# Performance work log

Hardware: AMD Instinct MI355X
Metric: run time of the kernel (lower is better)

Reference implementation:

```python
import jax, jax.numpy as jnp
import numpy as np

B, Q, K = 4, 1024, 2048
QDIM, MDIM, EDIM, H = 1024, 1024, 1024, 16
HD = EDIM // H

def setup_inputs() -> dict:
    key = jax.random.key(0)
    ks = jax.random.split(key, 7)
    s = lambda d: (1.0 / np.sqrt(d))
    return {
        'query': jax.random.normal(ks[0], (B, Q, QDIM), jnp.float32),
        'memory': jax.random.normal(ks[1], (B, K, MDIM), jnp.float32),
        'bias': jax.random.normal(ks[2], (B, K), jnp.float32),
        'Wq': jax.random.normal(ks[3], (QDIM, EDIM), jnp.float32) * s(QDIM),
        'Wk': jax.random.normal(ks[4], (MDIM, EDIM), jnp.float32) * s(MDIM),
        'Wv': jax.random.normal(ks[5], (MDIM, EDIM), jnp.float32) * s(MDIM),
        'Wo': jax.random.normal(ks[6], (EDIM, EDIM), jnp.float32) * s(EDIM),
    }

def reference(query, memory, bias, Wq, Wk, Wv, Wo):
    scale = HD ** -0.5
    # projections -> [B, H, Q/K, HD]
    q = (query @ Wq).reshape(B, Q, H, HD).transpose(0, 2, 1, 3)
    k = (memory @ Wk).reshape(B, K, H, HD).transpose(0, 2, 1, 3)
    v = (memory @ Wv).reshape(B, K, H, HD).transpose(0, 2, 1, 3)
    scores = jnp.einsum('bhqd,bhkd->bhqk', q, k) * scale
    scores = scores + bias[:, None, None, :]
    weights = jax.nn.softmax(scores, axis=-1)
    out = jnp.einsum('bhqk,bhkd->bhqd', weights, v)
    out = out.transpose(0, 2, 1, 3).reshape(B, Q, EDIM)
    return out @ Wo
```

## Files before the change

### kernel.cpp

```cpp
#include <hip/hip_runtime.h>
#include <cstdint>
#include <cstddef>

typedef unsigned short u16;
typedef __attribute__((ext_vector_type(8))) short bf16x8;
typedef __attribute__((ext_vector_type(4))) short bf16x4;
typedef __attribute__((ext_vector_type(4))) float f32x4;

#define B_  4
#define Q_  1024
#define K_  2048
#define E_  1024
#define H_  16
#define HD_ 64
#define LOG2E 1.4426950408889634f
#define M0_  16.0f

__device__ inline u16 f2bf(float f) {
  union { float f; uint32_t u; } x; x.f = f;
  return (u16)((x.u + 0x7fffu + ((x.u >> 16) & 1u)) >> 16);
}

__device__ inline short bfc(float f) {
  __bf16 h = (__bf16)f;
  return __builtin_bit_cast(short, h);
}

__device__ inline void gload16(const u16* g, void* l) {
  __builtin_amdgcn_global_load_lds((const __attribute__((address_space(1))) void*)g,
                                   (__attribute__((address_space(3))) void*)l, 16, 0, 0);
}

#define NQ8 (B_ * Q_ * E_ / 8)
#define NM8 (B_ * K_ * E_ / 8)
#define NBI (B_ * K_)
#define NPREP ((NQ8 + NM8 + NBI) / 256)
__global__ __launch_bounds__(256) void prep_all(const float* __restrict__ query,
                                                const float* __restrict__ memory,
                                                const float* __restrict__ bias,
                                                const float* W0, const float* W1,
                                                const float* W2, const float* W3,
                                                u16* __restrict__ qb,
                                                u16* __restrict__ mb,
                                                float* __restrict__ bias2,
                                                u16* T0, u16* T1, u16* T2, u16* T3) {
  __shared__ float t[64][65];
  int bid = blockIdx.x;
  if (bid < NPREP) {
    int i = bid * 256 + threadIdx.x;
    const float* src;
    u16* dst;
    if (i < NQ8) {
      src = query + (size_t)i * 8; dst = qb + (size_t)i * 8;
    } else if (i < NQ8 + NM8) {
      int j = i - NQ8;
      src = memory + (size_t)j * 8; dst = mb + (size_t)j * 8;
    } else {
      int j = i - (NQ8 + NM8);
      if (j < NBI) bias2[j] = bias[j] * LOG2E - M0_;
      return;
    }
    float4 a = *reinterpret_cast<const float4*>(src);
    float4 b = *reinterpret_cast<const float4*>(src + 4);
    union { u16 u[8]; uint4 v; } r;
    r.u[0] = f2bf(a.x); r.u[1] = f2bf(a.y); r.u[2] = f2bf(a.z); r.u[3] = f2bf(a.w);
    r.u[4] = f2bf(b.x); r.u[5] = f2bf(b.y); r.u[6] = f2bf(b.z); r.u[7] = f2bf(b.w);
    *reinterpret_cast<uint4*>(dst) = r.v;
  } else {
    int tb = bid - NPREP;
    int z = tb >> 8, xy = tb & 255;
    const float* W; u16* T;
    switch (z) {
      case 0: W = W0; T = T0; break;
      case 1: W = W1; T = T1; break;
      case 2: W = W2; T = T2; break;
      default: W = W3; T = T3; break;
    }
    int k0 = (xy & 15) * 64, n0 = (xy >> 4) * 64;
    int r = threadIdx.x >> 6, c = threadIdx.x & 63;
#pragma unroll
    for (int i = 0; i < 16; ++i)
      t[r + i * 4][c] = W[(size_t)(k0 + r + i * 4) * E_ + n0 + c];
    __syncthreads();
#pragma unroll
    for (int i = 0; i < 16; ++i)
      T[(size_t)(n0 + r + i * 4) * E_ + k0 + c] = f2bf(t[c][r + i * 4]);
  }
}

template <int MODE>
__device__ __forceinline__ void gemm_body(const u16* __restrict__ A,
                                          const u16* __restrict__ Bt,
                                          void* __restrict__ C,
                                          int M, int N, int Kc, int bx, int by,
                                          char* lds) {
  const int tid = threadIdx.x;
  const int w = tid >> 6, l = tid & 63;
  const int wr = w >> 1, wc = w & 1;
  const int lr = l & 15, lg = l >> 4;
  const int m0 = bx * 128, n0 = by * 128;

  const int e0g = tid * 8, e1g = e0g + 2048;
  const int row0 = e0g >> 5, row1 = e1g >> 5;
  const int lc0 = ((((e0g & 31) >> 3) ^ ((row0 >> 1) & 3)) * 8);
  const int lc1 = ((((e1g & 31) >> 3) ^ ((row1 >> 1) & 3)) * 8);
  const u16* Ar0 = A  + (size_t)(m0 + row0) * Kc + lc0;
  const u16* Ar1 = A  + (size_t)(m0 + row1) * Kc + lc1;
  const u16* Br0 = Bt + (size_t)(n0 + row0) * Kc + lc0;
  const u16* Br1 = Bt + (size_t)(n0 + row1) * Kc + lc1;
  const int d0 = tid * 16, d1 = d0 + 4096;

  const int ck = (lg ^ ((lr >> 1) & 3)) * 16;
  int aofs = (wr * 64 + lr) * 64 + ck;
  int bofs = 16384 + (wc * 64 + lr) * 64 + ck;

  f32x4 acc[4][4];
#pragma unroll
  for (int mt = 0; mt < 4; ++mt)
#pragma unroll
    for (int nt = 0; nt < 4; ++nt)
      acc[mt][nt] = (f32x4){0.f, 0.f, 0.f, 0.f};

  gload16(Ar0, lds + d0);
  gload16(Ar1, lds + d1);
  gload16(Br0, lds + 16384 + d0);
  gload16(Br1, lds + 16384 + d1);
  __syncthreads();

  const int NI = Kc >> 5;
  for (int ki = 0; ki < NI; ++ki) {
    if (ki + 1 < NI) {
      const int nb = ((ki & 1) ^ 1) * 8192;
      const int kk = (ki + 1) * 32;
      gload16(Ar0 + kk, lds + nb + d0);
      gload16(Ar1 + kk, lds + nb + d1);
      gload16(Br0 + kk, lds + 16384 + nb + d0);
      gload16(Br1 + kk, lds + 16384 + nb + d1);
    }

    bf16x8 a[4], b[4];
#pragma unroll
    for (int mt = 0; mt < 4; ++mt)
      a[mt] = *reinterpret_cast<const bf16x8*>(lds + aofs + mt * 1024);
#pragma unroll
    for (int nt = 0; nt < 4; ++nt)
      b[nt] = *reinterpret_cast<const bf16x8*>(lds + bofs + nt * 1024);
    __builtin_amdgcn_s_setprio(1);
#pragma unroll
    for (int mt = 0; mt < 4; ++mt)
#pragma unroll
      for (int nt = 0; nt < 4; ++nt)
        acc[mt][nt] = __builtin_amdgcn_mfma_f32_16x16x32_bf16(a[mt], b[nt], acc[mt][nt], 0, 0, 0);
    __builtin_amdgcn_s_setprio(0);

    aofs ^= 8192; bofs ^= 8192;
    __syncthreads();
  }

#pragma unroll
  for (int mt = 0; mt < 4; ++mt) {
#pragma unroll
    for (int nt = 0; nt < 4; ++nt) {
      int col = n0 + wc * 64 + nt * 16 + lr;
#pragma unroll
      for (int j = 0; j < 4; ++j) {
        int row = m0 + wr * 64 + mt * 16 + lg * 4 + j;
        float v = acc[mt][nt][j];
        if (MODE == 0) {
          ((float*)C)[(size_t)row * N + col] = v;
        } else if (MODE == 1) {
          ((u16*)C)[(size_t)row * N + col] = f2bf(v);
        } else if (MODE == 3) {
          ((u16*)C)[(size_t)row * N + col] = f2bf(v * (0.125f * LOG2E));
        } else {
          ((u16*)C)[((size_t)((col >> 11) * 16 + (row >> 6)) * 64 + (row & 63)) * 2048 + (col & 2047)] = f2bf(v);
        }
      }
    }
  }
}

__global__ __launch_bounds__(256) void gemm_out(const u16* __restrict__ A,
                                                const u16* __restrict__ Bt,
                                                void* __restrict__ C,
                                                int M, int N, int Kc) {
  __shared__ uint4 lds4[2048];
  int d = blockIdx.x;
  int bid = (d & 7) * 32 + (d >> 3);
  gemm_body<0>(A, Bt, C, M, N, Kc, bid >> 3, bid & 7, (char*)lds4);
}

__global__ __launch_bounds__(256) void proj_fused(const u16* __restrict__ qb,
                                                  const u16* __restrict__ mb,
                                                  const u16* __restrict__ wqt,
                                                  const u16* __restrict__ wkt,
                                                  const u16* __restrict__ wvt,
                                                  u16* __restrict__ qproj,
                                                  u16* __restrict__ kproj,
                                                  u16* __restrict__ vt) {
  __shared__ uint4 lds4[2048];
  char* lds = (char*)lds4;
  int d = blockIdx.x;
  int bid = (d & 7) * 160 + (d >> 3);
  if (bid < 256) {
    gemm_body<3>(qb, wqt, qproj, B_ * Q_, E_, E_, bid >> 3, bid & 7, lds);
  } else if (bid < 768) {
    int i = bid - 256;
    gemm_body<1>(mb, wkt, kproj, B_ * K_, E_, E_, i >> 3, i & 7, lds);
  } else {
    int i = bid - 768;
    gemm_body<2>(wvt, mb, vt, E_, B_ * K_, E_, i & 7, i >> 3, lds);
  }
}

__global__ __launch_bounds__(256, 4) void attn_kernel(const u16* __restrict__ qp,
                                                      const u16* __restrict__ kp,
                                                      const u16* __restrict__ vT,
                                                      const float* __restrict__ bias2,
                                                      u16* __restrict__ out) {
  __shared__ uint4 lds4[2048];
  char* ldsb = (char*)lds4;

  const int blk = blockIdx.x;
  const int hg = blk & 63, qt = blk >> 6;
  const int b = hg >> 4, h = hg & 15;
  const int tid = threadIdx.x;
  const int w = tid >> 6, l = tid & 63;
  const int lr = l & 15, lg = l >> 4;

  bf16x8 qfrag[2];
#pragma unroll
  for (int ks = 0; ks < 2; ++ks)
    qfrag[ks] = *reinterpret_cast<const bf16x8*>(
        qp + (size_t)(b * Q_ + qt * 64 + w * 16 + lr) * E_ + h * 64 + ks * 32 + lg * 8);

  f32x4 O[4];
  f32x4 Osum = (f32x4){0.f, 0.f, 0.f, 0.f};
#pragma unroll
  for (int ht = 0; ht < 4; ++ht) O[ht] = (f32x4){0.f, 0.f, 0.f, 0.f};
  const float* bias_b = bias2 + (size_t)b * K_;
  const u16* kbase = kp + (size_t)b * K_ * E_ + h * 64;
  const u16* vbase = vT + (size_t)(b * H_ + h) * HD_ * K_;

  const bf16x4 ones = {(short)0x3F80, (short)0x3F80, (short)0x3F80, (short)0x3F80};

  const int xk = (lr & 7) * 8;
  int kofs0 = lr * 128 + (((lg * 8) ^ xk) << 1);
  int kofs1 = lr * 128 + ((((32 + lg * 8)) ^ xk) << 1);
  int vofs[4];
#pragma unroll
  for (int ct = 0; ct < 4; ++ct)
    vofs[ct] = 16384 + lr * 128 + ((((ct * 16 + lg * 4)) ^ xk) << 1);

  const int e0 = tid * 8, e1 = e0 + 2048;
  const int r0 = e0 >> 6, r1 = e1 >> 6;
  const int sc0 = (e0 & 63) ^ ((r0 & 7) * 8);
  const int sc1 = (e1 & 63) ^ ((r1 & 7) * 8);

  gload16(kbase + (size_t)r0 * E_ + sc0, ldsb + tid * 16);
  gload16(kbase + (size_t)r1 * E_ + sc1, ldsb + 4096 + tid * 16);
  gload16(vbase + (size_t)r0 * K_ + sc0, ldsb + 16384 + tid * 16);
  gload16(vbase + (size_t)r1 * K_ + sc1, ldsb + 16384 + 4096 + tid * 16);
  __syncthreads();

  const int NT = K_ / 64;
  for (int t = 0; t < NT; ++t) {
    if (t + 1 < NT) {
      const int nb = ((t & 1) ^ 1) * 8192;
      int kk0 = (t + 1) * 64;
      gload16(kbase + (size_t)(kk0 + r0) * E_ + sc0, ldsb + nb + tid * 16);
      gload16(kbase + (size_t)(kk0 + r1) * E_ + sc1, ldsb + nb + 4096 + tid * 16);
      gload16(vbase + (size_t)r0 * K_ + kk0 + sc0, ldsb + 16384 + nb + tid * 16);
      gload16(vbase + (size_t)r1 * K_ + kk0 + sc1, ldsb + 16384 + nb + 4096 + tid * 16);
    }

    const float* bt = bias_b + t * 64;
    f32x4 S[4];
    __builtin_amdgcn_s_setprio(1);
#pragma unroll
    for (int ct = 0; ct < 4; ++ct) {
      bf16x8 kb0 = *reinterpret_cast<const bf16x8*>(ldsb + kofs0 + ct * 2048);
      bf16x8 kb1 = *reinterpret_cast<const bf16x8*>(ldsb + kofs1 + ct * 2048);
      float4 bv = *reinterpret_cast<const float4*>(&bt[ct * 16 + lg * 4]);
      f32x4 s; s[0] = bv.x; s[1] = bv.y; s[2] = bv.z; s[3] = bv.w;
      s = __builtin_amdgcn_mfma_f32_16x16x32_bf16(kb0, qfrag[0], s, 0, 0, 0);
      s = __builtin_amdgcn_mfma_f32_16x16x32_bf16(kb1, qfrag[1], s, 0, 0, 0);
      S[ct] = s;
    }
    __builtin_amdgcn_s_setprio(0);

    bf16x4 pf[4];
#pragma unroll
    for (int ct = 0; ct < 4; ++ct) {
      pf[ct][0] = bfc(exp2f(S[ct][0]));
      pf[ct][1] = bfc(exp2f(S[ct][1]));
      pf[ct][2] = bfc(exp2f(S[ct][2]));
      pf[ct][3] = bfc(exp2f(S[ct][3]));
    }

    __builtin_amdgcn_s_setprio(1);
#pragma unroll
    for (int ct = 0; ct < 4; ++ct) {
#pragma unroll
      for (int ht = 0; ht < 4; ++ht) {
        bf16x4 vb = *reinterpret_cast<const bf16x4*>(ldsb + vofs[ct] + ht * 2048);
        O[ht] = __builtin_amdgcn_mfma_f32_16x16x16bf16_1k(pf[ct], vb, O[ht], 0, 0, 0);
      }
      Osum = __builtin_amdgcn_mfma_f32_16x16x16bf16_1k(pf[ct], ones, Osum, 0, 0, 0);
    }
    __builtin_amdgcn_s_setprio(0);

    kofs0 ^= 8192; kofs1 ^= 8192;
#pragma unroll
    for (int ct = 0; ct < 4; ++ct) vofs[ct] ^= 8192;
    __syncthreads();
  }

#pragma unroll
  for (int j = 0; j < 4; ++j) {
    float inv = 1.f / Osum[j];
    int row = b * Q_ + qt * 64 + w * 16 + lg * 4 + j;
#pragma unroll
    for (int ht = 0; ht < 4; ++ht)
      out[(size_t)row * E_ + h * 64 + ht * 16 + lr] = (u16)bfc(O[ht][j] * inv);
  }
}

extern "C" void kernel_launch(void* const* d_in, const int* in_sizes, int n_in,
                              void* d_out, int out_size, void* d_ws, size_t ws_size,
                              hipStream_t stream) {
  const float* query  = (const float*)d_in[0];
  const float* memory = (const float*)d_in[1];
  const float* bias   = (const float*)d_in[2];
  const float* Wq     = (const float*)d_in[3];
  const float* Wk     = (const float*)d_in[4];
  const float* Wv     = (const float*)d_in[5];
  const float* Wo     = (const float*)d_in[6];
  float* out = (float*)d_out;

  char* p = (char*)d_ws;
  u16* qb    = (u16*)p; p += (size_t)B_ * Q_ * E_ * 2;
  u16* mb    = (u16*)p; p += (size_t)B_ * K_ * E_ * 2;
  u16* wqt   = (u16*)p; p += (size_t)E_ * E_ * 2;
  u16* wkt   = (u16*)p; p += (size_t)E_ * E_ * 2;
  u16* wvt   = (u16*)p; p += (size_t)E_ * E_ * 2;
  u16* wot   = (u16*)p; p += (size_t)E_ * E_ * 2;
  u16* qproj = (u16*)p; p += (size_t)B_ * Q_ * E_ * 2;
  u16* kproj = (u16*)p; p += (size_t)B_ * K_ * E_ * 2;
  u16* vt    = (u16*)p; p += (size_t)B_ * K_ * E_ * 2;
  u16* attn  = (u16*)p; p += (size_t)B_ * Q_ * E_ * 2;
  float* bias2 = (float*)p; p += (size_t)B_ * K_ * 4;

  prep_all<<<NPREP + 1024, 256, 0, stream>>>(query, memory, bias, Wq, Wk, Wv, Wo,
                                             qb, mb, bias2, wqt, wkt, wvt, wot);

  proj_fused<<<1280, 256, 0, stream>>>(qb, mb, wqt, wkt, wvt, qproj, kproj, vt);

  attn_kernel<<<B_ * H_ * (Q_ / 64), 256, 0, stream>>>(qproj, kproj, vt, bias2, attn);

  gemm_out<<<256, 256, 0, stream>>>(attn, wot, out, B_ * Q_, E_, E_);
}
```

Baseline: 152.4 us.

## Split attention key tiles across wave pairs with LDS reduction of partial outputs

Each wave now handles 32 query rows and half of each 64-key tile, instead of 16 query rows and the full tile. Each K and V fragment read from LDS therefore feeds two query sub-tiles, which halves LDS read traffic per MFMA. At the end, the two waves sharing the same queries combine their partial O and row sums through LDS before normalizing. The cost is more accumulator registers per wave, which may hurt occupancy under launch_bounds(256,4), plus an extra barrier and LDS exchange in the epilogue.

```diff
diff --git a/kernel.cpp b/kernel.cpp
--- a/kernel.cpp
+++ b/kernel.cpp
@@ -226,18 +226,25 @@
   const int b = hg >> 4, h = hg & 15;
   const int tid = threadIdx.x;
   const int w = tid >> 6, l = tid & 63;
+  const int wq = w & 1, wk = w >> 1;
   const int lr = l & 15, lg = l >> 4;
 
-  bf16x8 qfrag[2];
-#pragma unroll
-  for (int ks = 0; ks < 2; ++ks)
-    qfrag[ks] = *reinterpret_cast<const bf16x8*>(
-        qp + (size_t)(b * Q_ + qt * 64 + w * 16 + lr) * E_ + h * 64 + ks * 32 + lg * 8);
-
-  f32x4 O[4];
-  f32x4 Osum = (f32x4){0.f, 0.f, 0.f, 0.f};
-#pragma unroll
-  for (int ht = 0; ht < 4; ++ht) O[ht] = (f32x4){0.f, 0.f, 0.f, 0.f};
+  bf16x8 qfrag[2][2];
+#pragma unroll
+  for (int qi = 0; qi < 2; ++qi)
+#pragma unroll
+    for (int ks = 0; ks < 2; ++ks)
+      qfrag[ks][qi] = *reinterpret_cast<const bf16x8*>(
+          qp + (size_t)(b * Q_ + qt * 64 + wq * 32 + qi * 16 + lr) * E_ + h * 64 + ks * 32 + lg * 8);
+
+  f32x4 O[2][4];
+  f32x4 Osum[2];
+#pragma unroll
+  for (int qi = 0; qi < 2; ++qi) {
+    Osum[qi] = (f32x4){0.f, 0.f, 0.f, 0.f};
+#pragma unroll
+    for (int ht = 0; ht < 4; ++ht) O[qi][ht] = (f32x4){0.f, 0.f, 0.f, 0.f};
+  }
   const float* bias_b = bias2 + (size_t)b * K_;
   const u16* kbase = kp + (size_t)b * K_ * E_ + h * 64;
   const u16* vbase = vT + (size_t)(b * H_ + h) * HD_ * K_;
@@ -245,12 +252,12 @@
   const bf16x4 ones = {(short)0x3F80, (short)0x3F80, (short)0x3F80, (short)0x3F80};
 
   const int xk = (lr & 7) * 8;
-  int kofs0 = lr * 128 + (((lg * 8) ^ xk) << 1);
-  int kofs1 = lr * 128 + ((((32 + lg * 8)) ^ xk) << 1);
-  int vofs[4];
-#pragma unroll
-  for (int ct = 0; ct < 4; ++ct)
-    vofs[ct] = 16384 + lr * 128 + ((((ct * 16 + lg * 4)) ^ xk) << 1);
+  int kofs0 = (wk * 32 + lr) * 128 + (((lg * 8) ^ xk) << 1);
+  int kofs1 = (wk * 32 + lr) * 128 + ((((32 + lg * 8)) ^ xk) << 1);
+  int vofs[2];
+#pragma unroll
+  for (int ci = 0; ci < 2; ++ci)
+    vofs[ci] = 16384 + lr * 128 + ((((wk * 32 + ci * 16 + lg * 4)) ^ xk) << 1);
 
   const int e0 = tid * 8, e1 = e0 + 2048;
   const int r0 = e0 >> 6, r1 = e1 >> 6;
@@ -275,54 +282,89 @@
     }
 
     const float* bt = bias_b + t * 64;
-    f32x4 S[4];
+    f32x4 S[2][2];
     __builtin_amdgcn_s_setprio(1);
 #pragma unroll
-    for (int ct = 0; ct < 4; ++ct) {
-      bf16x8 kb0 = *reinterpret_cast<const bf16x8*>(ldsb + kofs0 + ct * 2048);
-      bf16x8 kb1 = *reinterpret_cast<const bf16x8*>(ldsb + kofs1 + ct * 2048);
-      float4 bv = *reinterpret_cast<const float4*>(&bt[ct * 16 + lg * 4]);
-      f32x4 s; s[0] = bv.x; s[1] = bv.y; s[2] = bv.z; s[3] = bv.w;
-      s = __builtin_amdgcn_mfma_f32_16x16x32_bf16(kb0, qfrag[0], s, 0, 0, 0);
-      s = __builtin_amdgcn_mfma_f32_16x16x32_bf16(kb1, qfrag[1], s, 0, 0, 0);
-      S[ct] = s;
+    for (int ci = 0; ci < 2; ++ci) {
+      bf16x8 kb0 = *reinterpret_cast<const bf16x8*>(ldsb + kofs0 + ci * 2048);
+      bf16x8 kb1 = *reinterpret_cast<const bf16x8*>(ldsb + kofs1 + ci * 2048);
+      float4 bv = *reinterpret_cast<const float4*>(&bt[wk * 32 + ci * 16 + lg * 4]);
+#pragma unroll
+      for (int qi = 0; qi < 2; ++qi) {
+        f32x4 s; s[0] = bv.x; s[1] = bv.y; s[2] = bv.z; s[3] = bv.w;
+        s = __builtin_amdgcn_mfma_f32_16x16x32_bf16(kb0, qfrag[0][qi], s, 0, 0, 0);
+        s = __builtin_amdgcn_mfma_f32_16x16x32_bf16(kb1, qfrag[1][qi], s, 0, 0, 0);
+        S[ci][qi] = s;
+      }
     }
     __builtin_amdgcn_s_setprio(0);
 
-    bf16x4 pf[4];
-#pragma unroll
-    for (int ct = 0; ct < 4; ++ct) {
-      pf[ct][0] = bfc(exp2f(S[ct][0]));
-      pf[ct][1] = bfc(exp2f(S[ct][1]));
-      pf[ct][2] = bfc(exp2f(S[ct][2]));
-      pf[ct][3] = bfc(exp2f(S[ct][3]));
-    }
+    bf16x4 pf[2][2];
+#pragma unroll
+    for (int ci = 0; ci < 2; ++ci)
+#pragma unroll
+      for (int qi = 0; qi < 2; ++qi) {
+        pf[ci][qi][0] = bfc(exp2f(S[ci][qi][0]));
+        pf[ci][qi][1] = bfc(exp2f(S[ci][qi][1]));
+        pf[ci][qi][2] = bfc(exp2f(S[ci][qi][2]));
+        pf[ci][qi][3] = bfc(exp2f(S[ci][qi][3]));
+      }
 
     __builtin_amdgcn_s_setprio(1);
 #pragma unroll
-    for (int ct = 0; ct < 4; ++ct) {
+    for (int ci = 0; ci < 2; ++ci) {
 #pragma unroll
       for (int ht = 0; ht < 4; ++ht) {
-        bf16x4 vb = *reinterpret_cast<const bf16x4*>(ldsb + vofs[ct] + ht * 2048);
-        O[ht] = __builtin_amdgcn_mfma_f32_16x16x16bf16_1k(pf[ct], vb, O[ht], 0, 0, 0);
-      }
-      Osum = __builtin_amdgcn_mfma_f32_16x16x16bf16_1k(pf[ct], ones, Osum, 0, 0, 0);
+        bf16x4 vb = *reinterpret_cast<const bf16x4*>(ldsb + vofs[ci] + ht * 2048);
+#pragma unroll
+        for (int qi = 0; qi < 2; ++qi)
+          O[qi][ht] = __builtin_amdgcn_mfma_f32_16x16x16bf16_1k(pf[ci][qi], vb, O[qi][ht], 0, 0, 0);
+      }
+#pragma unroll
+      for (int qi = 0; qi < 2; ++qi)
+        Osum[qi] = __builtin_amdgcn_mfma_f32_16x16x16bf16_1k(pf[ci][qi], ones, Osum[qi], 0, 0, 0);
     }
     __builtin_amdgcn_s_setprio(0);
 
     kofs0 ^= 8192; kofs1 ^= 8192;
-#pragma unroll
-    for (int ct = 0; ct < 4; ++ct) vofs[ct] ^= 8192;
+    vofs[0] ^= 8192; vofs[1] ^= 8192;
     __syncthreads();
   }
 
-#pragma unroll
-  for (int j = 0; j < 4; ++j) {
-    float inv = 1.f / Osum[j];
-    int row = b * Q_ + qt * 64 + w * 16 + lg * 4 + j;
-#pragma unroll
-    for (int ht = 0; ht < 4; ++ht)
-      out[(size_t)row * E_ + h * 64 + ht * 16 + lr] = (u16)bfc(O[ht][j] * inv);
+  float* ex = (float*)ldsb + ((size_t)(wq * 64 + l) * 44);
+  if (wk == 1) {
+#pragma unroll
+    for (int qi = 0; qi < 2; ++qi) {
+#pragma unroll
+      for (int ht = 0; ht < 4; ++ht)
+        *reinterpret_cast<f32x4*>(ex + qi * 16 + ht * 4) = O[qi][ht];
+      *reinterpret_cast<f32x4*>(ex + 32 + qi * 4) = Osum[qi];
+    }
+  }
+  __syncthreads();
+  if (wk == 0) {
+#pragma unroll
+    for (int qi = 0; qi < 2; ++qi) {
+#pragma unroll
+      for (int ht = 0; ht < 4; ++ht) {
+        f32x4 p = *reinterpret_cast<const f32x4*>(ex + qi * 16 + ht * 4);
+#pragma unroll
+        for (int j = 0; j < 4; ++j) O[qi][ht][j] += p[j];
+      }
+      f32x4 ps = *reinterpret_cast<const f32x4*>(ex + 32 + qi * 4);
+#pragma unroll
+      for (int j = 0; j < 4; ++j) Osum[qi][j] += ps[j];
+    }
+#pragma unroll
+    for (int qi = 0; qi < 2; ++qi)
+#pragma unroll
+      for (int j = 0; j < 4; ++j) {
+        float inv = 1.f / Osum[qi][j];
+        int row = b * Q_ + qt * 64 + wq * 32 + qi * 16 + lg * 4 + j;
+#pragma unroll
+        for (int ht = 0; ht < 4; ++ht)
+          out[(size_t)row * E_ + h * 64 + ht * 16 + lr] = (u16)bfc(O[qi][ht][j] * inv);
+      }
   }
 }
 
```

Result: faster. 149.0 us (-2.2%).

## Rework attention tile onto 32x32x16 MFMA with split-K across waves

Applied to the files above, without the earlier changes.

The attention kernel now uses 32x32x16 bf16 MFMAs instead of 16x16 ones. The four waves are split into two query halves and two key halves, and the K rows are permuted so the score accumulator layout feeds the P·V MFMA directly. The row sum is computed with a VALU reduction and a lane shuffle instead of an extra MFMA against ones, and P is packed with v_cvt_pk_bf16_f32. Partial O and sum from the two key-split waves are combined through LDS at the end. The aim is fewer, larger MFMAs and fewer LDS fragment reads per tile; the cost is an end-of-kernel reduction, higher register pressure, and only half the waves doing the final stores.

```diff
diff --git a/kernel.cpp b/kernel.cpp
--- a/kernel.cpp
+++ b/kernel.cpp
@@ -6,6 +6,7 @@
 typedef __attribute__((ext_vector_type(8))) short bf16x8;
 typedef __attribute__((ext_vector_type(4))) short bf16x4;
 typedef __attribute__((ext_vector_type(4))) float f32x4;
+typedef __attribute__((ext_vector_type(16))) float f32x16;
 
 #define B_  4
 #define Q_  1024
@@ -226,31 +227,39 @@
   const int b = hg >> 4, h = hg & 15;
   const int tid = threadIdx.x;
   const int w = tid >> 6, l = tid & 63;
-  const int lr = l & 15, lg = l >> 4;
-
-  bf16x8 qfrag[2];
-#pragma unroll
-  for (int ks = 0; ks < 2; ++ks)
-    qfrag[ks] = *reinterpret_cast<const bf16x8*>(
-        qp + (size_t)(b * Q_ + qt * 64 + w * 16 + lr) * E_ + h * 64 + ks * 32 + lg * 8);
-
-  f32x4 O[4];
-  f32x4 Osum = (f32x4){0.f, 0.f, 0.f, 0.f};
-#pragma unroll
-  for (int ht = 0; ht < 4; ++ht) O[ht] = (f32x4){0.f, 0.f, 0.f, 0.f};
+  const int wq = w & 1, wk = w >> 1;
+  const int l31 = l & 31, lh = l >> 5;
+
+  const int bk4 = l31 >> 2;
+  const int t4 = bk4 & 3;
+  const int pk31 = (((t4 == 1) || (t4 == 2)) ? (bk4 ^ 3) : bk4) * 4 + (l31 & 3);
+
+  bf16x8 qf[4];
+  const u16* qrow = qp + (size_t)(b * Q_ + qt * 64 + wq * 32 + l31) * E_ + h * 64 + lh * 8;
+#pragma unroll
+  for (int st = 0; st < 4; ++st)
+    qf[st] = *reinterpret_cast<const bf16x8*>(qrow + st * 16);
+
+  f32x16 O0, O1;
+#pragma unroll
+  for (int i = 0; i < 16; ++i) { O0[i] = 0.f; O1[i] = 0.f; }
+  float Osum = 0.f;
+
   const float* bias_b = bias2 + (size_t)b * K_;
   const u16* kbase = kp + (size_t)b * K_ * E_ + h * 64;
   const u16* vbase = vT + (size_t)(b * H_ + h) * HD_ * K_;
 
-  const bf16x4 ones = {(short)0x3F80, (short)0x3F80, (short)0x3F80, (short)0x3F80};
-
-  const int xk = (lr & 7) * 8;
-  int kofs0 = lr * 128 + (((lg * 8) ^ xk) << 1);
-  int kofs1 = lr * 128 + ((((32 + lg * 8)) ^ xk) << 1);
-  int vofs[4];
-#pragma unroll
-  for (int ct = 0; ct < 4; ++ct)
-    vofs[ct] = 16384 + lr * 128 + ((((ct * 16 + lg * 4)) ^ xk) << 1);
+  const int xkk = (pk31 & 7) * 8;
+  const int xvv = (l31 & 7) * 8;
+  int kofs[4];
+#pragma unroll
+  for (int st = 0; st < 4; ++st)
+    kofs[st] = (wk * 32 + pk31) * 128 + (((st * 16 + lh * 8) ^ xkk) << 1);
+  int vofs[2];
+#pragma unroll
+  for (int ksl = 0; ksl < 2; ++ksl)
+    vofs[ksl] = 16384 + l31 * 128 + (((wk * 32 + ksl * 16 + lh * 8) ^ xvv) << 1);
+  const float* bbase = bias_b + wk * 32 + lh * 8;
 
   const int e0 = tid * 8, e1 = e0 + 2048;
   const int r0 = e0 >> 6, r1 = e1 >> 6;
@@ -274,55 +283,85 @@
       gload16(vbase + (size_t)r1 * K_ + kk0 + sc1, ldsb + 16384 + nb + 4096 + tid * 16);
     }
 
-    const float* bt = bias_b + t * 64;
-    f32x4 S[4];
+    const float* bt = bbase + t * 64;
+    float4 bg0 = *reinterpret_cast<const float4*>(bt);
+    float4 bg1 = *reinterpret_cast<const float4*>(bt + 4);
+    float4 bg2 = *reinterpret_cast<const float4*>(bt + 16);
+    float4 bg3 = *reinterpret_cast<const float4*>(bt + 20);
+    f32x16 S;
+    S[0] = bg0.x; S[1] = bg0.y; S[2] = bg0.z; S[3] = bg0.w;
+    S[4] = bg1.x; S[5] = bg1.y; S[6] = bg1.z; S[7] = bg1.w;
+    S[8] = bg2.x; S[9] = bg2.y; S[10] = bg2.z; S[11] = bg2.w;
+    S[12] = bg3.x; S[13] = bg3.y; S[14] = bg3.z; S[15] = bg3.w;
     __builtin_amdgcn_s_setprio(1);
 #pragma unroll
-    for (int ct = 0; ct < 4; ++ct) {
-      bf16x8 kb0 = *reinterpret_cast<const bf16x8*>(ldsb + kofs0 + ct * 2048);
-      bf16x8 kb1 = *reinterpret_cast<const bf16x8*>(ldsb + kofs1 + ct * 2048);
-      float4 bv = *reinterpret_cast<const float4*>(&bt[ct * 16 + lg * 4]);
-      f32x4 s; s[0] = bv.x; s[1] = bv.y; s[2] = bv.z; s[3] = bv.w;
-      s = __builtin_amdgcn_mfma_f32_16x16x32_bf16(kb0, qfrag[0], s, 0, 0, 0);
-      s = __builtin_amdgcn_mfma_f32_16x16x32_bf16(kb1, qfrag[1], s, 0, 0, 0);
-      S[ct] = s;
+    for (int st = 0; st < 4; ++st) {
+      bf16x8 ka = *reinterpret_cast<const bf16x8*>(ldsb + kofs[st]);
+      S = __builtin_amdgcn_mfma_f32_32x32x16_bf16(ka, qf[st], S, 0, 0, 0);
     }
     __builtin_amdgcn_s_setprio(0);
 
-    bf16x4 pf[4];
-#pragma unroll
-    for (int ct = 0; ct < 4; ++ct) {
-      pf[ct][0] = bfc(exp2f(S[ct][0]));
-      pf[ct][1] = bfc(exp2f(S[ct][1]));
-      pf[ct][2] = bfc(exp2f(S[ct][2]));
-      pf[ct][3] = bfc(exp2f(S[ct][3]));
-    }
+#pragma unroll
+    for (int i = 0; i < 16; ++i) S[i] = exp2f(S[i]);
+    float ps = ((S[0] + S[1]) + (S[2] + S[3])) + ((S[4] + S[5]) + (S[6] + S[7]))
+             + ((S[8] + S[9]) + (S[10] + S[11])) + ((S[12] + S[13]) + (S[14] + S[15]));
+    ps += __shfl_xor(ps, 32, 64);
+    Osum += ps;
+
+    uint32_t u[8];
+#pragma unroll
+    for (int j = 0; j < 8; ++j) {
+      float plo = S[2 * j], phi = S[2 * j + 1];
+      asm("v_cvt_pk_bf16_f32 %0, %1, %2" : "=v"(u[j]) : "v"(plo), "v"(phi));
+    }
+    bf16x8 P0 = __builtin_bit_cast(bf16x8, (uint4){u[0], u[1], u[2], u[3]});
+    bf16x8 P1 = __builtin_bit_cast(bf16x8, (uint4){u[4], u[5], u[6], u[7]});
 
     __builtin_amdgcn_s_setprio(1);
-#pragma unroll
-    for (int ct = 0; ct < 4; ++ct) {
-#pragma unroll
-      for (int ht = 0; ht < 4; ++ht) {
-        bf16x4 vb = *reinterpret_cast<const bf16x4*>(ldsb + vofs[ct] + ht * 2048);
-        O[ht] = __builtin_amdgcn_mfma_f32_16x16x16bf16_1k(pf[ct], vb, O[ht], 0, 0, 0);
+    {
+      bf16x8 va;
+      va = *reinterpret_cast<const bf16x8*>(ldsb + vofs[0]);
+      O0 = __builtin_amdgcn_mfma_f32_32x32x16_bf16(va, P0, O0, 0, 0, 0);
+      va = *reinterpret_cast<const bf16x8*>(ldsb + vofs[0] + 4096);
+      O1 = __builtin_amdgcn_mfma_f32_32x32x16_bf16(va, P0, O1, 0, 0, 0);
+      va = *reinterpret_cast<const bf16x8*>(ldsb + vofs[1]);
+      O0 = __builtin_amdgcn_mfma_f32_32x32x16_bf16(va, P1, O0, 0, 0, 0);
+      va = *reinterpret_cast<const bf16x8*>(ldsb + vofs[1] + 4096);
+      O1 = __builtin_amdgcn_mfma_f32_32x32x16_bf16(va, P1, O1, 0, 0, 0);
+    }
+    __builtin_amdgcn_s_setprio(0);
+
+    kofs[0] ^= 8192; kofs[1] ^= 8192; kofs[2] ^= 8192; kofs[3] ^= 8192;
+    vofs[0] ^= 8192; vofs[1] ^= 8192;
+    __syncthreads();
+  }
+
+  float* ex = (float*)ldsb + (size_t)(wq * 64 + l) * 33;
+  if (wk == 1) {
+#pragma unroll
+    for (int i = 0; i < 16; ++i) ex[i] = O0[i];
+#pragma unroll
+    for (int i = 0; i < 16; ++i) ex[16 + i] = O1[i];
+    ex[32] = Osum;
+  }
+  __syncthreads();
+  if (wk == 0) {
+#pragma unroll
+    for (int i = 0; i < 16; ++i) O0[i] += ex[i];
+#pragma unroll
+    for (int i = 0; i < 16; ++i) O1[i] += ex[16 + i];
+    Osum += ex[32];
+    float inv = 1.f / Osum;
+    u16* orow = out + (size_t)(b * Q_ + qt * 64 + wq * 32 + l31) * E_ + h * 64;
+#pragma unroll
+    for (int g = 0; g < 4; ++g) {
+      int hd0 = 8 * g + 4 * lh;
+#pragma unroll
+      for (int j = 0; j < 4; ++j) {
+        orow[hd0 + j] = (u16)bfc(O0[4 * g + j] * inv);
+        orow[32 + hd0 + j] = (u16)bfc(O1[4 * g + j] * inv);
       }
-      Osum = __builtin_amdgcn_mfma_f32_16x16x16bf16_1k(pf[ct], ones, Osum, 0, 0, 0);
-    }
-    __builtin_amdgcn_s_setprio(0);
-
-    kofs0 ^= 8192; kofs1 ^= 8192;
-#pragma unroll
-    for (int ct = 0; ct < 4; ++ct) vofs[ct] ^= 8192;
-    __syncthreads();
-  }
-
-#pragma unroll
-  for (int j = 0; j < 4; ++j) {
-    float inv = 1.f / Osum[j];
-    int row = b * Q_ + qt * 64 + w * 16 + lg * 4 + j;
-#pragma unroll
-    for (int ht = 0; ht < 4; ++ht)
-      out[(size_t)row * E_ + h * 64 + ht * 16 + lr] = (u16)bfc(O[ht][j] * inv);
+    }
   }
 }
 
```

Result: faster. 148.7 us (-2.4%).
